# Kernel optimization log

Measured on AMD Instinct MI355X. Metric: run time of the kernel, lower is better.

The kernel has to match this reference:

```python
import jax, jax.numpy as jnp
import numpy as np
from jax import lax

TAGS = 27
START = 25
STOP = 26
HID = 512


def _conv2d(x, w, b, stride):
    # x: [N,1,H,W], w: [O,1,kh,kw]
    y = lax.conv_general_dilated(x, w, stride, 'VALID',
                                 dimension_numbers=('NCHW', 'OIHW', 'NCHW'))
    return y + b[None, :, None, None]


def _lstm_dir(x, wih, whh, bih, bhh):
    # x: [T, D] -> hs: [T, H]; PyTorch gate order i,f,g,o
    H = whh.shape[1]
    gx = x @ wih.T + (bih + bhh)  # [T, 4H] precomputed input contribution

    def step(carry, g_t):
        h, c = carry
        g = g_t + h @ whh.T
        i, f, gg, o = jnp.split(g, 4)
        c = jax.nn.sigmoid(f) * c + jax.nn.sigmoid(i) * jnp.tanh(gg)
        h = jax.nn.sigmoid(o) * jnp.tanh(c)
        return (h, c), h

    z = jnp.zeros((H,), x.dtype)
    _, hs = lax.scan(step, (z, z), gx)
    return hs


def _bilstm_layer(x, wf, uf, bf, bbf, wr, ur, br, bbr):
    fwd = _lstm_dir(x, wf, uf, bf, bbf)
    bwd = _lstm_dir(x[::-1], wr, ur, br, bbr)[::-1]
    return jnp.concatenate([fwd, bwd], axis=-1)  # [T, 2H]


def _feats(features,
           conv1_w, conv1_b, conv3_w, conv3_b, conv5_w, conv5_b,
           wih0f, whh0f, bih0f, bhh0f, wih0r, whh0r, bih0r, bhh0r,
           wih1f, whh1f, bih1f, bhh1f, wih1r, whh1r, bih1r, bhh1r,
           h2t_w, h2t_b):
    T = features.shape[0]
    nd = 4  # num_divisions
    out1 = _conv2d(features[:, :, :, 0:12 * nd], conv1_w, conv1_b, (1, nd))
    out3 = _conv2d(features[:, :, :, 0:14 * nd], conv3_w, conv3_b, (1, nd))
    out5 = _conv2d(features[:, :, :, 0:16 * nd], conv5_w, conv5_b, (1, nd))
    x = jnp.concatenate([out1.reshape(T, -1), out3.reshape(T, -1),
                         out5.reshape(T, -1)], axis=1)  # [T, 1728]
    x = _bilstm_layer(x, wih0f, whh0f, bih0f, bhh0f, wih0r, whh0r, bih0r, bhh0r)
    x = _bilstm_layer(x, wih1f, whh1f, bih1f, bhh1f, wih1r, whh1r, bih1r, bhh1r)
    return x @ h2t_w.T + h2t_b  # [T, TAGS]


def _viterbi(feats, transitions):
    init = jnp.full((TAGS,), -10000.0, feats.dtype).at[START].set(0.0)

    def step(fv, feat):
        # scores[next, prev] = fv[prev] + transitions[next, prev]
        scores = fv[None, :] + transitions
        bptr = jnp.argmax(scores, axis=1)
        fv_new = jnp.max(scores, axis=1) + feat
        return fv_new, bptr

    fv, bptrs = lax.scan(step, init, feats)
    terminal = fv + transitions[STOP]
    best_last = jnp.argmax(terminal)
    path_score = terminal[best_last]

    def back(tag, bp):
        return bp[tag], tag

    _, best_path = lax.scan(back, best_last, bptrs, reverse=True)
    return path_score, best_path


def setup_inputs() -> dict:
    key = jax.random.key(0)
    ks = jax.random.split(key, 40)
    T, C, D = 8192, 16, 1728

    def rn(k, shape, scale=0.05):
        return jax.random.normal(k, shape, jnp.float32) * scale

    inp = {
        'features': jax.random.normal(ks[0], (T, 1, 7, 64), jnp.float32),
        'conv1_w': rn(ks[1], (C, 1, 7, 4)), 'conv1_b': rn(ks[2], (C,)),
        'conv3_w': rn(ks[3], (C, 1, 4, 12)), 'conv3_b': rn(ks[4], (C,)),
        'conv5_w': rn(ks[5], (C, 1, 4, 20)), 'conv5_b': rn(ks[6], (C,)),
    }
    idx = 7
    dims = [D, 2 * HID]
    for l in range(2):
        for d in ('f', 'r'):
            inp[f'wih{l}{d}'] = rn(ks[idx], (4 * HID, dims[l])); idx += 1
            inp[f'whh{l}{d}'] = rn(ks[idx], (4 * HID, HID)); idx += 1
            inp[f'bih{l}{d}'] = rn(ks[idx], (4 * HID,)); idx += 1
            inp[f'bhh{l}{d}'] = rn(ks[idx], (4 * HID,)); idx += 1
    inp['h2t_w'] = rn(ks[idx], (TAGS, 2 * HID)); idx += 1
    inp['h2t_b'] = rn(ks[idx], (TAGS,)); idx += 1
    trans = jax.random.normal(ks[idx], (TAGS, TAGS), jnp.float32)
    trans = trans.at[START, :].set(-10000.0).at[:, STOP].set(-10000.0)
    inp['transitions'] = trans
    return inp


def reference(features,
              conv1_w, conv1_b, conv3_w, conv3_b, conv5_w, conv5_b,
              wih0f, whh0f, bih0f, bhh0f, wih0r, whh0r, bih0r, bhh0r,
              wih1f, whh1f, bih1f, bhh1f, wih1r, whh1r, bih1r, bhh1r,
              h2t_w, h2t_b, transitions):
    feats = _feats(features,
                   conv1_w, conv1_b, conv3_w, conv3_b, conv5_w, conv5_b,
                   wih0f, whh0f, bih0f, bhh0f, wih0r, whh0r, bih0r, bhh0r,
                   wih1f, whh1f, bih1f, bhh1f, wih1r, whh1r, bih1r, bhh1r,
                   h2t_w, h2t_b)
    score, path = _viterbi(feats, transitions)
    return score, path
```

## Files before the change

kernel.cpp:

```cpp
#include <hip/hip_runtime.h>
#include <cstdint>
#include <cstddef>

typedef unsigned short u16;
typedef unsigned int u32;
typedef unsigned char u8;
typedef short short8 __attribute__((ext_vector_type(8)));
typedef float f32x4 __attribute__((ext_vector_type(4)));

#define T_SEQ 8192
#define NTAGS 27
#define START_TAG 25
#define STOP_TAG 26
#define POISON 0xAAAAAAAAu
#define CHUNKS 8
#define CLEN 1024
#define WARM 64
#define SMAX (CLEN + WARM)

__device__ __forceinline__ float b2f(u16 b) {
    u32 u = ((u32)b) << 16; float f; __builtin_memcpy(&f, &u, 4); return f;
}
__device__ __forceinline__ u16 f2b(float f) {
    u32 u; __builtin_memcpy(&u, &f, 4);
    u32 lsb = (u >> 16) & 1u; u += 0x7fffu + lsb; return (u16)(u >> 16);
}
__device__ __forceinline__ float fsig(float x) { return 1.0f / (1.0f + __expf(-x)); }
__device__ __forceinline__ float ftanhf(float x) {
    float e = __expf(2.0f * x); return 1.0f - 2.0f / (e + 1.0f);
}

__global__ void cvt_bf16(const float* __restrict__ src, u16* __restrict__ dst, int n) {
    int i = blockIdx.x * 256 + threadIdx.x;
    if (i < n) dst[i] = f2b(src[i]);
}

__global__ void poison_k(uint4* __restrict__ p, int n4) {
    int i = blockIdx.x * 256 + threadIdx.x;
    if (i < n4) p[i] = make_uint4(POISON, POISON, POISON, POISON);
}

__global__ __launch_bounds__(256) void conv_feats(
    const float* __restrict__ feat,
    const float* __restrict__ c1w, const float* __restrict__ c1b,
    const float* __restrict__ c3w, const float* __restrict__ c3b,
    const float* __restrict__ c5w, const float* __restrict__ c5b,
    u16* __restrict__ xb)
{
    __shared__ float fl[448];
    __shared__ float w1[448], w3[768], w5[1280];
    __shared__ float b1[16], b3[16], b5[16];
    int t = blockIdx.x, tid = threadIdx.x;
    for (int i = tid; i < 448; i += 256) fl[i] = feat[(size_t)t * 448 + i];
    for (int i = tid; i < 448; i += 256) w1[i] = c1w[i];
    for (int i = tid; i < 768; i += 256) w3[i] = c3w[i];
    for (int i = tid; i < 1280; i += 256) w5[i] = c5w[i];
    if (tid < 16) { b1[tid] = c1b[tid]; b3[tid] = c3b[tid]; b5[tid] = c5b[tid]; }
    __syncthreads();
    for (int o = tid; o < 1728; o += 256) {
        float s;
        if (o < 192) {
            int c = o / 12, w = o % 12;
            s = b1[c];
            #pragma unroll
            for (int kh = 0; kh < 7; ++kh)
                #pragma unroll
                for (int kw = 0; kw < 4; ++kw)
                    s += fl[kh * 64 + w * 4 + kw] * w1[c * 28 + kh * 4 + kw];
        } else if (o < 960) {
            int o3 = o - 192; int c = o3 / 48, h = (o3 % 48) / 12, w = o3 % 12;
            s = b3[c];
            #pragma unroll
            for (int kh = 0; kh < 4; ++kh)
                #pragma unroll
                for (int kw = 0; kw < 12; ++kw)
                    s += fl[(h + kh) * 64 + w * 4 + kw] * w3[c * 48 + kh * 12 + kw];
        } else {
            int o5 = o - 960; int c = o5 / 48, h = (o5 % 48) / 12, w = o5 % 12;
            s = b5[c];
            #pragma unroll
            for (int kh = 0; kh < 4; ++kh)
                #pragma unroll
                for (int kw = 0; kw < 20; ++kw)
                    s += fl[(h + kh) * 64 + w * 4 + kw] * w5[c * 80 + kh * 20 + kw];
        }
        xb[(size_t)t * 1728 + o] = f2b(s);
    }
}

__global__ __launch_bounds__(256, 2) void gemm_bt(
    const u16* __restrict__ A,
    const u16* __restrict__ B0, const u16* __restrict__ B1,
    const float* __restrict__ bi0, const float* __restrict__ bh0,
    const float* __restrict__ bi1, const float* __restrict__ bh1,
    u16* __restrict__ C, int M, int K)
{
    int dir = blockIdx.z;
    const u16* B = dir ? B1 : B0;
    const float* bi = dir ? bi1 : bi0;
    const float* bh = dir ? bh1 : bh0;
    __shared__ u16 As[128 * 32];
    __shared__ u16 Bs[128 * 32];
    int tid = threadIdx.x;
    int tileM = blockIdx.x * 128, tileN = blockIdx.y * 128;
    int wave = tid >> 6, lane = tid & 63;
    int wm = (wave & 1) * 64, wn = (wave >> 1) * 64;
    int m16 = lane & 15, quad = lane >> 4;
    f32x4 acc[4][4] = {};
    for (int k0 = 0; k0 < K; k0 += 32) {
        #pragma unroll
        for (int p = 0; p < 2; ++p) {
            int cid = p * 256 + tid;
            int row = cid >> 2, ck = (cid & 3) * 8;
            *(uint4*)(&As[row * 32 + ck]) = *(const uint4*)(&A[(size_t)(tileM + row) * K + k0 + ck]);
            *(uint4*)(&Bs[row * 32 + ck]) = *(const uint4*)(&B[(size_t)(tileN + row) * K + k0 + ck]);
        }
        __syncthreads();
        short8 af[4], bfr[4];
        #pragma unroll
        for (int i = 0; i < 4; ++i) af[i] = *(const short8*)(&As[(wm + i * 16 + m16) * 32 + quad * 8]);
        #pragma unroll
        for (int i = 0; i < 4; ++i) bfr[i] = *(const short8*)(&Bs[(wn + i * 16 + m16) * 32 + quad * 8]);
        #pragma unroll
        for (int im = 0; im < 4; ++im)
            #pragma unroll
            for (int in = 0; in < 4; ++in)
                acc[im][in] = __builtin_amdgcn_mfma_f32_16x16x32_bf16(af[im], bfr[in], acc[im][in], 0, 0, 0);
        __syncthreads();
    }
    size_t dbase = (size_t)dir * M * 2048;
    #pragma unroll
    for (int im = 0; im < 4; ++im)
        #pragma unroll
        for (int in = 0; in < 4; ++in) {
            int col = tileN + wn + in * 16 + m16;
            float bias = bi[col] + bh[col];
            #pragma unroll
            for (int r = 0; r < 4; ++r) {
                int row = tileM + wm + im * 16 + quad * 4 + r;
                C[dbase + (size_t)row * 2048 + col] = f2b(acc[im][in][r] + bias);
            }
        }
}

__global__ __launch_bounds__(256) void lstm_rec(
    const u16* __restrict__ gx,
    u16* __restrict__ hb,
    const float* __restrict__ whh_f,
    const float* __restrict__ whh_r,
    u32* __restrict__ ex)
{
    int bid = blockIdx.x;
    int dir = bid >> 8;
    int chunk = (bid >> 5) & 7;
    int blk = bid & 31;
    const float* whh = dir ? whh_r : whh_f;
    int tid = threadIdx.x;
    int a = tid & 15, q = tid >> 4;
    int base16 = blk * 16;

    __shared__ float h_lds[512];
    __shared__ float p2[1024];

    float4 wreg[4][8];
    #pragma unroll
    for (int rr = 0; rr < 4; ++rr) {
        int rl = 4 * a + rr;
        int grow = (rl >> 4) * 512 + base16 + (rl & 15);
        const float* wp = &whh[(size_t)grow * 512 + q * 32];
        #pragma unroll
        for (int ff = 0; ff < 8; ++ff) {
            int f = ((ff + q) & 7);
            wreg[rr][ff] = *(const float4*)(wp + f * 4);
        }
    }
    for (int i = tid; i < 512; i += 256) h_lds[i] = 0.0f;
    __syncthreads();

    int warm = dir ? ((chunk == CHUNKS - 1) ? 0 : WARM)
                   : ((chunk == 0) ? 0 : WARM);
    int nsteps = CLEN + warm;
    int t0 = dir ? (chunk * CLEN + CLEN - 1 + warm) : (chunk * CLEN - warm);
    u32* exs = ex + (size_t)(dir * CHUNKS + chunk) * (SMAX * 256);

    size_t dirT = (size_t)dir * T_SEQ;
    float c_reg = 0.0f;
    int growme = (tid >> 4) * 512 + base16 + (tid & 15);
    float gxv = 0.0f;
    if (tid < 64) gxv = b2f(gx[(dirT + t0) * 2048 + growme]);

    for (int s = 0; s < nsteps; ++s) {
        int t = dir ? (t0 - s) : (t0 + s);
        float gxn = 0.0f;
        if (s + 1 < nsteps && tid < 64) {
            int tn = dir ? (t - 1) : (t + 1);
            gxn = b2f(gx[(dirT + tn) * 2048 + growme]);
        }
        {
            float4 hreg[8];
            #pragma unroll
            for (int ff = 0; ff < 8; ++ff) {
                int f = ((ff + q) & 7);
                hreg[ff] = *(const float4*)(&h_lds[q * 32 + f * 4]);
            }
            float a0 = 0.f, a1 = 0.f, a2 = 0.f, a3 = 0.f;
            #pragma unroll
            for (int ff = 0; ff < 8; ++ff) {
                float4 h4 = hreg[ff];
                a0 += wreg[0][ff].x * h4.x + wreg[0][ff].y * h4.y + wreg[0][ff].z * h4.z + wreg[0][ff].w * h4.w;
                a1 += wreg[1][ff].x * h4.x + wreg[1][ff].y * h4.y + wreg[1][ff].z * h4.z + wreg[1][ff].w * h4.w;
                a2 += wreg[2][ff].x * h4.x + wreg[2][ff].y * h4.y + wreg[2][ff].z * h4.z + wreg[2][ff].w * h4.w;
                a3 += wreg[3][ff].x * h4.x + wreg[3][ff].y * h4.y + wreg[3][ff].z * h4.z + wreg[3][ff].w * h4.w;
            }
            *(float4*)(&p2[(q * 16 + a) * 4]) = make_float4(a0, a1, a2, a3);
        }
        __syncthreads();
        if (tid < 64) {
            int g = tid;
            float red = gxv;
            #pragma unroll
            for (int qq = 0; qq < 16; ++qq)
                red += p2[(qq * 16 + (g >> 2)) * 4 + (g & 3)];
            int u = g & 15;
            float iv = __shfl(red, u, 64);
            float fv = __shfl(red, u + 16, 64);
            float gv = __shfl(red, u + 32, 64);
            float ov = __shfl(red, u + 48, 64);
            float c = fsig(fv) * c_reg + fsig(iv) * ftanhf(gv);
            float h = fsig(ov) * ftanhf(c);
            c_reg = c;
            float h0 = __shfl(h, 2 * g, 64);
            float h1 = __shfl(h, 2 * g + 1, 64);
            if (g < 8) {
                u32 w = (u32)f2b(h0) | ((u32)f2b(h1) << 16);
                if (w == POISON) w ^= 1u;
                __hip_atomic_store(&exs[s * 256 + blk * 8 + g], w,
                                   __ATOMIC_RELAXED, __HIP_MEMORY_SCOPE_AGENT);
                if (s >= warm) {
                    u32* ho = (u32*)hb + (size_t)t * 512 + dir * 256 + blk * 8 + g;
                    *ho = w;
                }
            }
            if (s + 1 < nsteps) {
                const u32* hw = &exs[s * 256 + 4 * g];
                u32 v0 = POISON, v1 = POISON, v2 = POISON, v3 = POISON;
                int spins = 0;
                do {
                    if (v0 == POISON) v0 = __hip_atomic_load(hw + 0, __ATOMIC_RELAXED, __HIP_MEMORY_SCOPE_AGENT);
                    if (v1 == POISON) v1 = __hip_atomic_load(hw + 1, __ATOMIC_RELAXED, __HIP_MEMORY_SCOPE_AGENT);
                    if (v2 == POISON) v2 = __hip_atomic_load(hw + 2, __ATOMIC_RELAXED, __HIP_MEMORY_SCOPE_AGENT);
                    if (v3 == POISON) v3 = __hip_atomic_load(hw + 3, __ATOMIC_RELAXED, __HIP_MEMORY_SCOPE_AGENT);
                    if (++spins > (1 << 16)) break;
                } while ((v0 == POISON) | (v1 == POISON) | (v2 == POISON) | (v3 == POISON));
                float* hd = &h_lds[8 * g];
                hd[0] = b2f((u16)(v0 & 0xffffu)); hd[1] = b2f((u16)(v0 >> 16));
                hd[2] = b2f((u16)(v1 & 0xffffu)); hd[3] = b2f((u16)(v1 >> 16));
                hd[4] = b2f((u16)(v2 & 0xffffu)); hd[5] = b2f((u16)(v2 >> 16));
                hd[6] = b2f((u16)(v3 & 0xffffu)); hd[7] = b2f((u16)(v3 >> 16));
            }
            gxv = gxn;
        }
        __syncthreads();
    }
}

__global__ __launch_bounds__(256) void h2t_feats(
    const u16* __restrict__ hb1,
    const float* __restrict__ w,
    const float* __restrict__ b,
    float* __restrict__ feats)
{
    int t = blockIdx.x * 4 + (threadIdx.x >> 6);
    int l = threadIdx.x & 63;
    int n = l & 31, jh = l >> 5;
    float s = 0.f;
    if (n < NTAGS) {
        const float* wr = &w[n * 1024 + jh * 512];
        const u16* hr = &hb1[(size_t)t * 1024 + jh * 512];
        for (int j = 0; j < 512; j += 8) {
            uint4 hv = *(const uint4*)(&hr[j]);
            float4 w0 = *(const float4*)(&wr[j]);
            float4 w1 = *(const float4*)(&wr[j + 4]);
            s += b2f((u16)(hv.x & 0xffffu)) * w0.x + b2f((u16)(hv.x >> 16)) * w0.y
               + b2f((u16)(hv.y & 0xffffu)) * w0.z + b2f((u16)(hv.y >> 16)) * w0.w
               + b2f((u16)(hv.z & 0xffffu)) * w1.x + b2f((u16)(hv.z >> 16)) * w1.y
               + b2f((u16)(hv.w & 0xffffu)) * w1.z + b2f((u16)(hv.w >> 16)) * w1.w;
        }
    }
    s += __shfl_xor(s, 32, 64);
    if (n < NTAGS && jh == 0) feats[t * 32 + n] = s + b[n];
}

#define VCLEN 256
#define VCHUNKS 32
#define VWARM 128

__global__ __launch_bounds__(64) void vit_fwd(
    const float* __restrict__ feats,
    const float* __restrict__ trans,
    u8* __restrict__ bptr,
    float* __restrict__ fvfin)
{
    __shared__ float tr_lds[NTAGS * NTAGS];
    __shared__ float fch[(VCLEN + VWARM) * 32];
    int c = blockIdx.x, l = threadIdx.x;
    int warm = (c == 0) ? 0 : VWARM;
    int t0 = c * VCLEN - warm;
    int nst = VCLEN + warm;
    for (int i = l; i < NTAGS * NTAGS; i += 64) tr_lds[i] = trans[i];
    for (int i = l * 4; i < nst * 32; i += 64 * 4)
        *(float4*)(&fch[i]) = *(const float4*)(&feats[(size_t)t0 * 32 + i]);
    __syncthreads();
    float trn[NTAGS];
    int lc = (l < NTAGS) ? l : 0;
    #pragma unroll
    for (int p = 0; p < NTAGS; ++p) trn[p] = tr_lds[lc * NTAGS + p];
    float fv = (c == 0) ? ((l == START_TAG) ? 0.f : -10000.f) : 0.f;
    for (int s = 0; s < nst; ++s) {
        float fvv[NTAGS];
        #pragma unroll
        for (int p = 0; p < NTAGS; ++p) fvv[p] = __shfl(fv, p, 64);
        float m0 = fvv[0] + trn[0]; int i0 = 0;
        float m1 = fvv[7] + trn[7]; int i1 = 7;
        float m2 = fvv[14] + trn[14]; int i2 = 14;
        float m3 = fvv[21] + trn[21]; int i3 = 21;
        #pragma unroll
        for (int p = 1; p < 7; ++p) { float sc = fvv[p] + trn[p]; if (sc > m0) { m0 = sc; i0 = p; } }
        #pragma unroll
        for (int p = 8; p < 14; ++p) { float sc = fvv[p] + trn[p]; if (sc > m1) { m1 = sc; i1 = p; } }
        #pragma unroll
        for (int p = 15; p < 21; ++p) { float sc = fvv[p] + trn[p]; if (sc > m2) { m2 = sc; i2 = p; } }
        #pragma unroll
        for (int p = 22; p < 27; ++p) { float sc = fvv[p] + trn[p]; if (sc > m3) { m3 = sc; i3 = p; } }
        if (m1 > m0) { m0 = m1; i0 = i1; }
        if (m3 > m2) { m2 = m3; i2 = i3; }
        if (m2 > m0) { m0 = m2; i0 = i2; }
        if (l < NTAGS) {
            fv = m0 + fch[s * 32 + l];
            if (s >= warm) bptr[(size_t)(t0 + s) * 32 + l] = (u8)i0;
        }
    }
    if (c == VCHUNKS - 1 && l < NTAGS) fvfin[l] = fv;
}

__global__ __launch_bounds__(64) void vit_back(
    const u8* __restrict__ bptr,
    u8* __restrict__ path_all,
    u8* __restrict__ maps)
{
    __shared__ u8 bp[VCLEN * 32];
    __shared__ u8 pa[VCLEN * 32];
    int c = blockIdx.x, l = threadIdx.x;
    for (int i = l * 16; i < VCLEN * 32; i += 64 * 16)
        *(uint4*)(&bp[i]) = *(const uint4*)(&bptr[(size_t)c * VCLEN * 32 + i]);
    __syncthreads();
    if (l < NTAGS) {
        int tag = l;
        for (int tt = VCLEN - 1; tt >= 0; --tt) {
            pa[tt * 32 + l] = (u8)tag;
            tag = bp[tt * 32 + tag];
        }
        maps[c * 32 + l] = (u8)tag;
    }
    __syncthreads();
    for (int i = l * 16; i < VCLEN * 32; i += 64 * 16)
        *(uint4*)(&path_all[(size_t)c * VCLEN * 32 + i]) = *(const uint4*)(&pa[i]);
}

__global__ __launch_bounds__(256) void vit_fin(
    const float* __restrict__ fvfin, const float* __restrict__ trans,
    const u8* __restrict__ maps, const u8* __restrict__ path_all,
    const float* __restrict__ feats, float* __restrict__ out)
{
    __shared__ float tr_l[NTAGS * NTAGS];
    __shared__ u8 entry[VCHUNKS];
    __shared__ u8 pal[T_SEQ];
    __shared__ float psum[256];
    int tid = threadIdx.x;
    for (int i = tid; i < NTAGS * NTAGS; i += 256) tr_l[i] = trans[i];
    __syncthreads();
    if (tid < 64) {
        int l = tid;
        float term = (l < NTAGS) ? fvfin[l] + tr_l[STOP_TAG * NTAGS + l] : -3.4e38f;
        int idx = l;
        #pragma unroll
        for (int off = 32; off > 0; off >>= 1) {
            float ot = __shfl_xor(term, off, 64);
            int oi = __shfl_xor(idx, off, 64);
            if (ot > term || (ot == term && oi < idx)) { term = ot; idx = oi; }
        }
        if (l == 0) {
            int tag = idx;
            for (int c = VCHUNKS - 1; c >= 0; --c) {
                entry[c] = (u8)tag;
                tag = maps[c * 32 + tag];
            }
        }
    }
    __syncthreads();
    for (int t = tid; t < T_SEQ; t += 256) {
        u8 p = path_all[(size_t)t * 32 + entry[t >> 8]];
        pal[t] = p;
        out[1 + t] = (float)p;
    }
    __syncthreads();
    float s = 0.f;
    for (int t = tid; t < T_SEQ; t += 256) {
        int pt = pal[t];
        int pp = (t == 0) ? START_TAG : (int)pal[t - 1];
        s += tr_l[pt * NTAGS + pp] + feats[(size_t)t * 32 + pt];
    }
    psum[tid] = s;
    __syncthreads();
    #pragma unroll
    for (int off = 128; off > 0; off >>= 1) {
        if (tid < off) psum[tid] += psum[tid + off];
        __syncthreads();
    }
    if (tid == 0)
        out[0] = psum[0] + tr_l[STOP_TAG * NTAGS + pal[T_SEQ - 1]];
}

extern "C" void kernel_launch(void* const* d_in, const int* in_sizes, int n_in,
                              void* d_out, int out_size, void* d_ws, size_t ws_size,
                              hipStream_t stream)
{
    (void)in_sizes; (void)n_in; (void)out_size; (void)ws_size;
    const float* features = (const float*)d_in[0];
    const float* c1w = (const float*)d_in[1];  const float* c1b = (const float*)d_in[2];
    const float* c3w = (const float*)d_in[3];  const float* c3b = (const float*)d_in[4];
    const float* c5w = (const float*)d_in[5];  const float* c5b = (const float*)d_in[6];
    const float* wih0f = (const float*)d_in[7];  const float* whh0f = (const float*)d_in[8];
    const float* bih0f = (const float*)d_in[9];  const float* bhh0f = (const float*)d_in[10];
    const float* wih0r = (const float*)d_in[11]; const float* whh0r = (const float*)d_in[12];
    const float* bih0r = (const float*)d_in[13]; const float* bhh0r = (const float*)d_in[14];
    const float* wih1f = (const float*)d_in[15]; const float* whh1f = (const float*)d_in[16];
    const float* bih1f = (const float*)d_in[17]; const float* bhh1f = (const float*)d_in[18];
    const float* wih1r = (const float*)d_in[19]; const float* whh1r = (const float*)d_in[20];
    const float* bih1r = (const float*)d_in[21]; const float* bhh1r = (const float*)d_in[22];
    const float* h2t_w = (const float*)d_in[23]; const float* h2t_b = (const float*)d_in[24];
    const float* trans = (const float*)d_in[25];

    char* ws = (char*)d_ws;
    u16* xb     = (u16*)(ws);
    u32* ex     = (u32*)(ws);
    u16* w0fb   = (u16*)(ws + 28311552);
    u16* w0rb   = (u16*)(ws + 35389440);
    u16* w1fb   = (u16*)(ws + 42467328);
    u16* w1rb   = (u16*)(ws + 46661632);
    u16* gx     = (u16*)(ws + 50855936);
    u16* hb0    = (u16*)(ws + 117964800);
    u16* hb1    = (u16*)(ws + 134742016);
    float* feats = (float*)(ws + 151519232);
    u8* bptr    = (u8*)(ws + 152567808);
    u8* path_all = (u8*)(ws + 50855936);
    u8* maps     = (u8*)(ws + 50855936 + 262144);
    float* fvfin = (float*)(ws + 50855936 + 263168);

    const int exWords = 2 * CHUNKS * SMAX * 256;
    const int exV4 = exWords / 4;

    cvt_bf16<<<(2048 * 1728 + 255) / 256, 256, 0, stream>>>(wih0f, w0fb, 2048 * 1728);
    cvt_bf16<<<(2048 * 1728 + 255) / 256, 256, 0, stream>>>(wih0r, w0rb, 2048 * 1728);
    cvt_bf16<<<(2048 * 1024 + 255) / 256, 256, 0, stream>>>(wih1f, w1fb, 2048 * 1024);
    cvt_bf16<<<(2048 * 1024 + 255) / 256, 256, 0, stream>>>(wih1r, w1rb, 2048 * 1024);

    conv_feats<<<T_SEQ, 256, 0, stream>>>(features, c1w, c1b, c3w, c3b, c5w, c5b, xb);

    dim3 g0(64, 16, 2);
    gemm_bt<<<g0, 256, 0, stream>>>(xb, w0fb, w0rb, bih0f, bhh0f, bih0r, bhh0r, gx, T_SEQ, 1728);
    poison_k<<<(exV4 + 255) / 256, 256, 0, stream>>>((uint4*)ex, exV4);
    lstm_rec<<<2 * CHUNKS * 32, 256, 0, stream>>>(gx, hb0, whh0f, whh0r, ex);

    gemm_bt<<<g0, 256, 0, stream>>>(hb0, w1fb, w1rb, bih1f, bhh1f, bih1r, bhh1r, gx, T_SEQ, 1024);
    poison_k<<<(exV4 + 255) / 256, 256, 0, stream>>>((uint4*)ex, exV4);
    lstm_rec<<<2 * CHUNKS * 32, 256, 0, stream>>>(gx, hb1, whh1f, whh1r, ex);

    h2t_feats<<<T_SEQ / 4, 256, 0, stream>>>(hb1, h2t_w, h2t_b, feats);

    vit_fwd<<<VCHUNKS, 64, 0, stream>>>(feats, trans, bptr, fvfin);
    vit_back<<<VCHUNKS, 64, 0, stream>>>(bptr, path_all, maps);
    vit_fin<<<1, 256, 0, stream>>>(fvfin, trans, maps, path_all, feats, (float*)d_out);
}
```

Before: 5.079 ms.

## Stream bf16-packed recurrent weights from memory instead of holding fp32 in registers

A new pack_whh kernel converts each LSTM direction's recurrent weight matrix to bf16 and reorders it so each thread's slice is contiguous and coalesced. lstm_rec no longer keeps 128 fp32 weights per thread in registers; it re-reads the packed bf16 weights from global memory (served from cache) every timestep and unpacks them with bit shifts. The aim is to free roughly 128 VGPRs and shorten the per-block prologue. In exchange, every step of the serial recurrence now waits on memory loads, and the recurrent weights lose precision by dropping to bf16.

After: 5.359 ms. +5.5%, slower.

```diff
diff --git a/kernel.cpp b/kernel.cpp
--- a/kernel.cpp
+++ b/kernel.cpp
@@ -25,6 +25,12 @@
     u32 u; __builtin_memcpy(&u, &f, 4);
     u32 lsb = (u >> 16) & 1u; u += 0x7fffu + lsb; return (u16)(u >> 16);
 }
+__device__ __forceinline__ float blo(u32 u) {
+    u32 v = u << 16; float f; __builtin_memcpy(&f, &v, 4); return f;
+}
+__device__ __forceinline__ float bhi(u32 u) {
+    u32 v = u & 0xffff0000u; float f; __builtin_memcpy(&f, &v, 4); return f;
+}
 __device__ __forceinline__ float fsig(float x) { return 1.0f / (1.0f + __expf(-x)); }
 __device__ __forceinline__ float ftanhf(float x) {
     float e = __expf(2.0f * x); return 1.0f - 2.0f / (e + 1.0f);
@@ -38,6 +44,30 @@
 __global__ void poison_k(uint4* __restrict__ p, int n4) {
     int i = blockIdx.x * 256 + threadIdx.x;
     if (i < n4) p[i] = make_uint4(POISON, POISON, POISON, POISON);
+}
+
+__global__ __launch_bounds__(256) void pack_whh(
+    const float* __restrict__ wf, const float* __restrict__ wr_,
+    uint4* __restrict__ wpk)
+{
+    int idx = blockIdx.x * 256 + threadIdx.x;
+    int tid = idx & 255;
+    int j   = (idx >> 8) & 15;
+    int blk = (idx >> 12) & 31;
+    int dir = (idx >> 17) & 1;
+    const float* src = dir ? wr_ : wf;
+    int a = tid & 15, q = tid >> 4;
+    int rr = j >> 2, fp = j & 3;
+    int rl = 4 * a + rr;
+    int grow = (rl >> 4) * 512 + blk * 16 + (rl & 15);
+    int f0 = ((2 * fp + q) & 7), f1 = ((2 * fp + 1 + q) & 7);
+    const float* wp = src + (size_t)grow * 512 + q * 32;
+    uint4 pk;
+    pk.x = (u32)f2b(wp[f0 * 4 + 0]) | ((u32)f2b(wp[f0 * 4 + 1]) << 16);
+    pk.y = (u32)f2b(wp[f0 * 4 + 2]) | ((u32)f2b(wp[f0 * 4 + 3]) << 16);
+    pk.z = (u32)f2b(wp[f1 * 4 + 0]) | ((u32)f2b(wp[f1 * 4 + 1]) << 16);
+    pk.w = (u32)f2b(wp[f1 * 4 + 2]) | ((u32)f2b(wp[f1 * 4 + 3]) << 16);
+    wpk[idx] = pk;
 }
 
 __global__ __launch_bounds__(256) void conv_feats(
@@ -146,15 +176,13 @@
 __global__ __launch_bounds__(256) void lstm_rec(
     const u16* __restrict__ gx,
     u16* __restrict__ hb,
-    const float* __restrict__ whh_f,
-    const float* __restrict__ whh_r,
+    const uint4* __restrict__ wpk,
     u32* __restrict__ ex)
 {
     int bid = blockIdx.x;
     int dir = bid >> 8;
     int chunk = (bid >> 5) & 7;
     int blk = bid & 31;
-    const float* whh = dir ? whh_r : whh_f;
     int tid = threadIdx.x;
     int a = tid & 15, q = tid >> 4;
     int base16 = blk * 16;
@@ -162,18 +190,8 @@
     __shared__ float h_lds[512];
     __shared__ float p2[1024];
 
-    float4 wreg[4][8];
-    #pragma unroll
-    for (int rr = 0; rr < 4; ++rr) {
-        int rl = 4 * a + rr;
-        int grow = (rl >> 4) * 512 + base16 + (rl & 15);
-        const float* wp = &whh[(size_t)grow * 512 + q * 32];
-        #pragma unroll
-        for (int ff = 0; ff < 8; ++ff) {
-            int f = ((ff + q) & 7);
-            wreg[rr][ff] = *(const float4*)(wp + f * 4);
-        }
-    }
+    const uint4* wb = wpk + (size_t)(dir * 32 + blk) * 16 * 256;
+
     for (int i = tid; i < 512; i += 256) h_lds[i] = 0.0f;
     __syncthreads();
 
@@ -197,20 +215,24 @@
             gxn = b2f(gx[(dirT + tn) * 2048 + growme]);
         }
         {
-            float4 hreg[8];
-            #pragma unroll
-            for (int ff = 0; ff < 8; ++ff) {
-                int f = ((ff + q) & 7);
-                hreg[ff] = *(const float4*)(&h_lds[q * 32 + f * 4]);
-            }
             float a0 = 0.f, a1 = 0.f, a2 = 0.f, a3 = 0.f;
             #pragma unroll
-            for (int ff = 0; ff < 8; ++ff) {
-                float4 h4 = hreg[ff];
-                a0 += wreg[0][ff].x * h4.x + wreg[0][ff].y * h4.y + wreg[0][ff].z * h4.z + wreg[0][ff].w * h4.w;
-                a1 += wreg[1][ff].x * h4.x + wreg[1][ff].y * h4.y + wreg[1][ff].z * h4.z + wreg[1][ff].w * h4.w;
-                a2 += wreg[2][ff].x * h4.x + wreg[2][ff].y * h4.y + wreg[2][ff].z * h4.z + wreg[2][ff].w * h4.w;
-                a3 += wreg[3][ff].x * h4.x + wreg[3][ff].y * h4.y + wreg[3][ff].z * h4.z + wreg[3][ff].w * h4.w;
+            for (int fp = 0; fp < 4; ++fp) {
+                int f0 = ((2 * fp + q) & 7), f1 = ((2 * fp + 1 + q) & 7);
+                float4 hA = *(const float4*)(&h_lds[q * 32 + f0 * 4]);
+                float4 hB = *(const float4*)(&h_lds[q * 32 + f1 * 4]);
+                uint4 w0 = wb[(0 * 4 + fp) * 256 + tid];
+                uint4 w1 = wb[(1 * 4 + fp) * 256 + tid];
+                uint4 w2 = wb[(2 * 4 + fp) * 256 + tid];
+                uint4 w3 = wb[(3 * 4 + fp) * 256 + tid];
+                a0 += blo(w0.x) * hA.x + bhi(w0.x) * hA.y + blo(w0.y) * hA.z + bhi(w0.y) * hA.w
+                    + blo(w0.z) * hB.x + bhi(w0.z) * hB.y + blo(w0.w) * hB.z + bhi(w0.w) * hB.w;
+                a1 += blo(w1.x) * hA.x + bhi(w1.x) * hA.y + blo(w1.y) * hA.z + bhi(w1.y) * hA.w
+                    + blo(w1.z) * hB.x + bhi(w1.z) * hB.y + blo(w1.w) * hB.z + bhi(w1.w) * hB.w;
+                a2 += blo(w2.x) * hA.x + bhi(w2.x) * hA.y + blo(w2.y) * hA.z + bhi(w2.y) * hA.w
+                    + blo(w2.z) * hB.x + bhi(w2.z) * hB.y + blo(w2.w) * hB.z + bhi(w2.w) * hB.w;
+                a3 += blo(w3.x) * hA.x + bhi(w3.x) * hA.y + blo(w3.y) * hA.z + bhi(w3.y) * hA.w
+                    + blo(w3.z) * hB.x + bhi(w3.z) * hB.y + blo(w3.w) * hB.z + bhi(w3.w) * hB.w;
             }
             *(float4*)(&p2[(q * 16 + a) * 4]) = make_float4(a0, a1, a2, a3);
         }
@@ -444,6 +466,7 @@
     char* ws = (char*)d_ws;
     u16* xb     = (u16*)(ws);
     u32* ex     = (u32*)(ws);
+    uint4* wpk  = (uint4*)(ws + 18874368);
     u16* w0fb   = (u16*)(ws + 28311552);
     u16* w0rb   = (u16*)(ws + 35389440);
     u16* w1fb   = (u16*)(ws + 42467328);
@@ -470,11 +493,13 @@
     dim3 g0(64, 16, 2);
     gemm_bt<<<g0, 256, 0, stream>>>(xb, w0fb, w0rb, bih0f, bhh0f, bih0r, bhh0r, gx, T_SEQ, 1728);
     poison_k<<<(exV4 + 255) / 256, 256, 0, stream>>>((uint4*)ex, exV4);
-    lstm_rec<<<2 * CHUNKS * 32, 256, 0, stream>>>(gx, hb0, whh0f, whh0r, ex);
+    pack_whh<<<1024, 256, 0, stream>>>(whh0f, whh0r, wpk);
+    lstm_rec<<<2 * CHUNKS * 32, 256, 0, stream>>>(gx, hb0, wpk, ex);
 
     gemm_bt<<<g0, 256, 0, stream>>>(hb0, w1fb, w1rb, bih1f, bhh1f, bih1r, bhh1r, gx, T_SEQ, 1024);
     poison_k<<<(exV4 + 255) / 256, 256, 0, stream>>>((uint4*)ex, exV4);
-    lstm_rec<<<2 * CHUNKS * 32, 256, 0, stream>>>(gx, hb1, whh1f, whh1r, ex);
+    pack_whh<<<1024, 256, 0, stream>>>(whh1f, whh1r, wpk);
+    lstm_rec<<<2 * CHUNKS * 32, 256, 0, stream>>>(gx, hb1, wpk, ex);
 
     h2t_feats<<<T_SEQ / 4, 256, 0, stream>>>(hb1, h2t_w, h2t_b, feats);
 
```
